# Kernel tuning notes

Measured on AMD Instinct MI355X. Metric: run time of the kernel, lower is better.

## Reference

```python
import jax, jax.numpy as jnp
import numpy as np

N_NODES = 100000
N_EDGES = 3200000
IN_FEAT = 128
HIDDEN = 32
NUM_LAYERS = 4
K = 35
NODES_PER_GRAPH = 100


def setup_inputs() -> dict:
    key = jax.random.key(0)
    ks = jax.random.split(key, 20)
    inp = {}
    inp['x'] = jax.random.normal(ks[0], (N_NODES, IN_FEAT), dtype=jnp.float32)
    inp['edge_index'] = jax.random.randint(ks[1], (2, N_EDGES), 0, N_NODES, dtype=jnp.int64)
    inp['batch'] = (jnp.arange(N_NODES, dtype=jnp.int64) // NODES_PER_GRAPH)
    # GCNConv weights (PyG: lin weight [in, out], bias [out])
    dims = [IN_FEAT] + [HIDDEN] * NUM_LAYERS
    for i in range(NUM_LAYERS):
        s = 1.0 / np.sqrt(dims[i])
        inp[f'w{i}'] = jax.random.normal(ks[2 + i], (dims[i], HIDDEN), dtype=jnp.float32) * s
        inp[f'b{i}'] = jnp.zeros((HIDDEN,), dtype=jnp.float32)
    # head: Conv1d(128->16,k=1), Conv1d(16->32,k=5), fc1(416->128), fc2(128->1)
    inp['conv1_w'] = jax.random.normal(ks[8], (16, HIDDEN * NUM_LAYERS, 1), dtype=jnp.float32) * (1.0 / np.sqrt(128))
    inp['conv1_b'] = jnp.zeros((16,), dtype=jnp.float32)
    inp['conv2_w'] = jax.random.normal(ks[9], (32, 16, 5), dtype=jnp.float32) * (1.0 / np.sqrt(16 * 5))
    inp['conv2_b'] = jnp.zeros((32,), dtype=jnp.float32)
    lin_in = 32 * (K // 2 - 4)  # 416
    inp['fc1_w'] = jax.random.normal(ks[10], (128, lin_in), dtype=jnp.float32) * (1.0 / np.sqrt(lin_in))
    inp['fc1_b'] = jnp.zeros((128,), dtype=jnp.float32)
    inp['fc2_w'] = jax.random.normal(ks[11], (1, 128), dtype=jnp.float32) * (1.0 / np.sqrt(128))
    inp['fc2_b'] = jnp.zeros((1,), dtype=jnp.float32)
    return inp


def _gcn_conv(x, w, b, src, dst, n):
    # PyG GCNConv: h = x @ W; add self-loops; sym-normalized scatter-add; + bias
    h = x @ w
    deg = jnp.ones((n,), h.dtype).at[dst].add(1.0)  # degree incl. self-loop
    dis = jax.lax.rsqrt(deg)
    coef = dis[src] * dis[dst]  # [E]
    agg = jax.ops.segment_sum(h[src] * coef[:, None], dst, num_segments=n)
    return agg + h / deg[:, None] + b  # self-loop norm = 1/deg


def reference(x, edge_index, batch, w0, b0, w1, b1, w2, b2, w3, b3,
              conv1_w, conv1_b, conv2_w, conv2_b, fc1_w, fc1_b, fc2_w, fc2_b):
    src, dst = edge_index[0], edge_index[1]
    n = x.shape[0]
    xs = []
    h = x
    for w, b in ((w0, b0), (w1, b1), (w2, b2), (w3, b3)):
        h = jnp.tanh(_gcn_conv(h, w, b, src, dst, n))
        xs.append(h)
    feat = jnp.concatenate(xs, axis=1)  # [N, 128]
    # global_sort_pool: graphs are contiguous blocks of NODES_PER_GRAPH nodes
    G = n // NODES_PER_GRAPH
    dense = feat.reshape(G, NODES_PER_GRAPH, -1)
    order = jnp.argsort(-dense[:, :, -1], axis=1)  # descending by last channel
    topk = jnp.take_along_axis(dense, order[:, :, None], axis=1)[:, :K]  # [G,K,128]
    y = topk.transpose(0, 2, 1)  # [G,128,K]
    y = jax.nn.relu(jnp.einsum('oc,gck->gok', conv1_w[:, :, 0], y) + conv1_b[None, :, None])
    L = y.shape[-1] // 2  # MaxPool1d(2), drop trailing element
    y = y[..., :L * 2].reshape(G, 16, L, 2).max(axis=-1)  # [G,16,17]
    y = jax.lax.conv_general_dilated(y, conv2_w, (1,), 'VALID',
                                     dimension_numbers=('NCH', 'OIH', 'NCH'))
    y = jax.nn.relu(y + conv2_b[None, :, None])  # [G,32,13]
    y = y.reshape(G, -1)  # [G,416]
    y = jax.nn.relu(y @ fc1_w.T + fc1_b)  # dropout is identity in eval
    return jax.nn.sigmoid(y @ fc2_w.T + fc2_b)  # [G,1]
```

## Files before the change

kernel.cpp:

```cpp
#include <hip/hip_runtime.h>
#include <hip/hip_fp16.h>
#include <math.h>

#define N_NODES 100000
#define N_EDGES 3200000
#define HIDDEN 32
#define K_TOP 35
#define NPG 100
#define N_GRAPHS 1000

#define BSHIFT 9
#define NLOC 512
#define NBUCK 196
#define CAP 17408
#define NBB 1024
#define BIN_CHUNK 13


__global__ void k_bin(const int* __restrict__ src, const int* __restrict__ dst,
                      int* __restrict__ bcnt, unsigned int* __restrict__ bdata) {
    __shared__ int h[NBUCK];
    __shared__ int lbase[NBUCK];
    __shared__ int lcur[NBUCK];
    int t = threadIdx.x;
    for (int i = t; i < NBUCK; i += 256) { h[i] = 0; lcur[i] = 0; }
    __syncthreads();
    int base = blockIdx.x * (256 * BIN_CHUNK);
    int ss[BIN_CHUNK], ds[BIN_CHUNK];
#pragma unroll
    for (int k = 0; k < BIN_CHUNK; k++) {
        int e = base + k * 256 + t;
        if (e < N_EDGES) {
            ss[k] = src[e];
            ds[k] = dst[e];
            atomicAdd(&h[ds[k] >> BSHIFT], 1);
        } else ds[k] = -1;
    }
    __syncthreads();
    for (int i = t; i < NBUCK; i += 256)
        lbase[i] = h[i] ? atomicAdd(&bcnt[i], h[i]) : 0;
    __syncthreads();
#pragma unroll
    for (int k = 0; k < BIN_CHUNK; k++) {
        int d = ds[k];
        if (d >= 0) {
            int bk = d >> BSHIFT;
            int pos = atomicAdd(&lcur[bk], 1);
            bdata[bk * CAP + lbase[bk] + pos] =
                ((unsigned int)ss[k] << BSHIFT) | (unsigned int)(d & (NLOC - 1));
        }
    }
}

__global__ void k_build(const unsigned int* __restrict__ bdata, const int* __restrict__ bcnt,
                        int2* __restrict__ rc, float* __restrict__ dis,
                        int* __restrict__ csr) {
    __shared__ int h[NLOC];
    __shared__ int sd[NLOC];
    __shared__ int rp[NLOC];
    __shared__ int cur[NLOC];
    int b = blockIdx.x, t = threadIdx.x;
    if (t < NLOC) h[t] = 0;
    __syncthreads();
    int r0 = b * CAP, r1 = r0 + bcnt[b];
    for (int i = r0 + t; i < r1; i += 1024)
        atomicAdd(&h[bdata[i] & (NLOC - 1)], 1);
    __syncthreads();
    int v = (t < NLOC) ? h[t] : 0;
    if (t < NLOC) sd[t] = v;
    __syncthreads();
    for (int off = 1; off < NLOC; off <<= 1) {
        int x = (t >= off && t < NLOC) ? sd[t - off] : 0;
        __syncthreads();
        if (t < NLOC) sd[t] += x;
        __syncthreads();
    }
    if (t < NLOC) {
        int excl = sd[t] - v;
        int node = (b << BSHIFT) + t;
        rp[t] = r0 + excl;
        cur[t] = 0;
        if (node < N_NODES) {
            rc[node] = make_int2(r0 + excl, v);
            dis[node] = rsqrtf((float)(v + 1));
        }
    }
    __syncthreads();
    for (int i = r0 + t; i < r1; i += 1024) {
        unsigned int u = bdata[i];
        int loc = u & (NLOC - 1);
        int pos = atomicAdd(&cur[loc], 1);
        csr[rp[loc] + pos] = (int)(u >> BSHIFT);
    }
}


__global__ void k_mm0(const float* __restrict__ in, const float* __restrict__ w,
                      const float* __restrict__ dis, char* __restrict__ hs) {
    __shared__ float wl[128 * HIDDEN];
    int t = threadIdx.x;
    for (int i = t; i < 128 * HIDDEN; i += 256) wl[i] = w[i];
    __syncthreads();
    int n0 = blockIdx.x * 512 + t;
    int n1 = n0 + 256;
    bool has0 = n0 < N_NODES, has1 = n1 < N_NODES;
    int m0 = has0 ? n0 : 0, m1 = has1 ? n1 : 0;
    const float* r0p = in + (size_t)m0 * 128;
    const float* r1p = in + (size_t)m1 * 128;
    float acc0[HIDDEN], acc1[HIDDEN];
#pragma unroll
    for (int o = 0; o < HIDDEN; o++) { acc0[o] = 0.f; acc1[o] = 0.f; }
    for (int c4 = 0; c4 < 32; c4++) {
        float4 va = *(const float4*)(r0p + c4 * 4);
        float4 vb = *(const float4*)(r1p + c4 * 4);
        float xa[4] = {va.x, va.y, va.z, va.w};
        float xb[4] = {vb.x, vb.y, vb.z, vb.w};
#pragma unroll
        for (int k = 0; k < 4; k++) {
            const float* wr = &wl[(c4 * 4 + k) * HIDDEN];
#pragma unroll
            for (int o = 0; o < HIDDEN; o++) {
                float wv = wr[o];
                acc0[o] += xa[k] * wv;
                acc1[o] += xb[k] * wv;
            }
        }
    }
    if (has0) {
        float d = dis[m0];
        float4* hr = (float4*)(hs + (size_t)m0 * 64);
#pragma unroll
        for (int qq = 0; qq < 4; qq++) {
            __half2 p[4];
#pragma unroll
            for (int k = 0; k < 4; k++)
                p[k] = __floats2half2_rn(acc0[8 * qq + 2 * k] * d, acc0[8 * qq + 2 * k + 1] * d);
            hr[qq] = *(float4*)p;
        }
    }
    if (has1) {
        float d = dis[m1];
        float4* hr = (float4*)(hs + (size_t)m1 * 64);
#pragma unroll
        for (int qq = 0; qq < 4; qq++) {
            __half2 p[4];
#pragma unroll
            for (int k = 0; k < 4; k++)
                p[k] = __floats2half2_rn(acc1[8 * qq + 2 * k] * d, acc1[8 * qq + 2 * k + 1] * d);
            hr[qq] = *(float4*)p;
        }
    }
}

__global__ void k_agg(const float4* __restrict__ hs4, const float* __restrict__ dis,
                      const int2* __restrict__ rc, const int* __restrict__ csr_src,
                      const float* __restrict__ bias,
                      float* __restrict__ feat, int col_off,
                      const float* __restrict__ wnext, char* __restrict__ hsn) {
    __shared__ float wl[32 * 33];
    __shared__ float tv[8][36];
    int tt = threadIdx.x;
    if (wnext) {
        for (int i = tt; i < 1024; i += 256)
            wl[(i >> 5) * 33 + (i & 31)] = wnext[i];
    }
    __syncthreads();
    int n = (blockIdx.x * 256 + tt) >> 5;
    int c = tt & 31;
    int r = c & 3;
    int ph = c >> 2;
    int slot = tt >> 5;
    int2 rcv = rc[n];
    int start = rcv.x, m = rcv.y;
    float d = dis[n];
    float4 sv = hs4[(size_t)n * 4 + r];
    float aA[8] = {0.f, 0.f, 0.f, 0.f, 0.f, 0.f, 0.f, 0.f};
    float aB[8] = {0.f, 0.f, 0.f, 0.f, 0.f, 0.f, 0.f, 0.f};

    for (int base = 0; base < m; base += 32) {
        int e = base + c;
        int idx = (e < m) ? __builtin_nontemporal_load(csr_src + start + e) : N_NODES;
        int id0 = __shfl(idx, ph, 32);
        int id1 = __shfl(idx, 8 + ph, 32);
        int id2 = __shfl(idx, 16 + ph, 32);
        int id3 = __shfl(idx, 24 + ph, 32);
        float4 g0 = hs4[(size_t)id0 * 4 + r];
        float4 g1 = hs4[(size_t)id1 * 4 + r];
        float4 g2 = hs4[(size_t)id2 * 4 + r];
        float4 g3 = hs4[(size_t)id3 * 4 + r];
        const __half2* h0 = (const __half2*)&g0;
        const __half2* h1 = (const __half2*)&g1;
        const __half2* h2 = (const __half2*)&g2;
        const __half2* h3 = (const __half2*)&g3;
        float2 f;
#pragma unroll
        for (int j = 0; j < 4; j++) {
            f = __half22float2(h0[j]); aA[2 * j] += f.x; aA[2 * j + 1] += f.y;
        }
#pragma unroll
        for (int j = 0; j < 4; j++) {
            f = __half22float2(h1[j]); aB[2 * j] += f.x; aB[2 * j + 1] += f.y;
        }
#pragma unroll
        for (int j = 0; j < 4; j++) {
            f = __half22float2(h2[j]); aA[2 * j] += f.x; aA[2 * j + 1] += f.y;
        }
#pragma unroll
        for (int j = 0; j < 4; j++) {
            f = __half22float2(h3[j]); aB[2 * j] += f.x; aB[2 * j + 1] += f.y;
        }
    }
    float s[8];
#pragma unroll
    for (int k = 0; k < 8; k++) {
        float v = aA[k] + aB[k];
        v += __shfl_xor(v, 4);
        v += __shfl_xor(v, 8);
        v += __shfl_xor(v, 16);
        s[k] = v;
    }
    float s01 = (ph & 1) ? s[1] : s[0];
    float s23 = (ph & 1) ? s[3] : s[2];
    float s45 = (ph & 1) ? s[5] : s[4];
    float s67 = (ph & 1) ? s[7] : s[6];
    float s03 = (ph & 2) ? s23 : s01;
    float s47 = (ph & 2) ? s67 : s45;
    float sp  = (ph & 4) ? s47 : s03;
    const __half2* sh = (const __half2*)&sv;
    __half2 q01 = (ph & 2) ? sh[1] : sh[0];
    __half2 q23 = (ph & 2) ? sh[3] : sh[2];
    __half2 qq  = (ph & 4) ? q23 : q01;
    float self = (ph & 1) ? __high2float(qq) : __low2float(qq);
    float bv = bias[8 * r + ph];
    float ov = tanhf(d * (sp + self) + bv);
    __builtin_nontemporal_store(ov, &feat[(size_t)n * 128 + col_off + 8 * r + ph]);
    if (wnext) {
        tv[slot][8 * r + ph] = ov;
        __builtin_amdgcn_wave_barrier();
        float o = 0.f;
#pragma unroll 8
        for (int k = 0; k < 32; k++)
            o += tv[slot][k] * wl[k * 33 + c];
        o *= d;
        float oh = __shfl_xor(o, 1);
        if ((c & 1) == 0) {
            __half2 pck = __floats2half2_rn(o, oh);
            *(__half2*)(hsn + (size_t)n * 64 + (size_t)c * 2) = pck;
        }
    }
}


__global__ void __launch_bounds__(256, 4)
k_head(const float* __restrict__ feat,
       const float* __restrict__ c1w, const float* __restrict__ c1b,
       const float* __restrict__ c2w, const float* __restrict__ c2b,
       const float* __restrict__ f1w, const float* __restrict__ f1b,
       const float* __restrict__ f2w, const float* __restrict__ f2b,
       float* __restrict__ out) {
    __shared__ float vals[NPG];
    __shared__ int sel[K_TOP];
    __shared__ float tk[K_TOP * 132];
    __shared__ float wl1[16 * 129];
    __shared__ float y1[16][36];
    __shared__ float y2[16][17];
    __shared__ float y3[416];
    __shared__ float y4[128];
    __shared__ float r2[128];
    int g = blockIdx.x, t = threadIdx.x;
    const float* fg = feat + (size_t)g * NPG * 128;

    for (int i = t; i < 2048; i += 256)
        wl1[(i >> 7) * 129 + (i & 127)] = c1w[i];
    if (t < NPG) vals[t] = fg[t * 128 + 127];
    __syncthreads();
    if (t < NPG) {
        float v = vals[t];
        int r = 0;
        for (int j = 0; j < NPG; j++) {
            float u = vals[j];
            r += (u > v) || (u == v && j < t);
        }
        if (r < K_TOP) sel[r] = t;
    }
    __syncthreads();
    for (int i = t; i < K_TOP * 32; i += 256) {
        int k = i >> 5, c4 = i & 31;
        *(float4*)&tk[k * 132 + 4 * c4] = *(const float4*)&fg[sel[k] * 128 + 4 * c4];
    }
    __syncthreads();
    for (int i = t; i < 16 * K_TOP; i += 256) {
        int o = i & 15, k = i >> 4;
        float s = c1b[o];
        const float* wr = &wl1[o * 129];
        const float* xr = &tk[k * 132];
#pragma unroll 8
        for (int c = 0; c < 128; c++) s += wr[c] * xr[c];
        y1[o][k] = fmaxf(s, 0.f);
    }
    __syncthreads();
    for (int i = t; i < 16 * 17; i += 256) {
        int o = i & 15, l = i >> 4;
        y2[o][l] = fmaxf(y1[o][2 * l], y1[o][2 * l + 1]);
    }
    __syncthreads();
    for (int idx = t; idx < 32 * 13; idx += 256) {
        int o2 = idx / 13, ttp = idx - o2 * 13;
        float s = c2b[o2];
        const float* wr = c2w + o2 * 80;
#pragma unroll
        for (int i = 0; i < 16; i++)
#pragma unroll
            for (int j = 0; j < 5; j++) s += wr[i * 5 + j] * y2[i][ttp + j];
        y3[idx] = fmaxf(s, 0.f);
    }
    __syncthreads();
    {
        int o = t >> 1, h = t & 1;
        const float4* wr4 = (const float4*)(f1w + o * 416) + h * 52;
        const float* yb = y3 + h * 208;
        float s = 0.f;
#pragma unroll 4
        for (int i = 0; i < 52; i++) {
            float4 w4 = wr4[i];
            s += w4.x * yb[4 * i] + w4.y * yb[4 * i + 1] +
                 w4.z * yb[4 * i + 2] + w4.w * yb[4 * i + 3];
        }
        s += __shfl_xor(s, 1);
        if (h == 0) y4[o] = fmaxf(s + f1b[o], 0.f);
    }
    __syncthreads();
    if (t < 128) r2[t] = f2w[t] * y4[t];
    __syncthreads();
    for (int off = 64; off > 0; off >>= 1) {
        if (t < off) r2[t] += r2[t + off];
        __syncthreads();
    }
    if (t == 0) out[g] = 1.0f / (1.0f + expf(-(r2[0] + f2b[0])));
}


static inline size_t alignup(size_t x) { return (x + 255) & ~(size_t)255; }

extern "C" void kernel_launch(void* const* d_in, const int* in_sizes, int n_in,
                              void* d_out, int out_size, void* d_ws, size_t ws_size,
                              hipStream_t stream) {
    const float* x    = (const float*)d_in[0];
    const int*   ei   = (const int*)d_in[1];
    const int*   srcp = ei;
    const int*   dstp = ei + N_EDGES;
    const float* w0 = (const float*)d_in[3];
    const float* b0 = (const float*)d_in[4];
    const float* w1 = (const float*)d_in[5];
    const float* b1 = (const float*)d_in[6];
    const float* w2 = (const float*)d_in[7];
    const float* b2 = (const float*)d_in[8];
    const float* w3 = (const float*)d_in[9];
    const float* b3 = (const float*)d_in[10];
    const float* c1w = (const float*)d_in[11];
    const float* c1b = (const float*)d_in[12];
    const float* c2w = (const float*)d_in[13];
    const float* c2b = (const float*)d_in[14];
    const float* f1w = (const float*)d_in[15];
    const float* f1b = (const float*)d_in[16];
    const float* f2w = (const float*)d_in[17];
    const float* f2b = (const float*)d_in[18];
    float* out = (float*)d_out;

    char* p = (char*)d_ws;
    int2* rcv    = (int2*)p; p += alignup(sizeof(int2) * N_NODES);
    float* dis   = (float*)p; p += alignup(sizeof(float) * N_NODES);
    int* bcnt    = (int*)p; p += alignup(sizeof(int) * NBUCK);
    int* csr     = (int*)p; p += alignup(sizeof(int) * (size_t)NBUCK * CAP);
    char* U = p;
    unsigned int* bdata = (unsigned int*)U;
    char* hsA = U;
    char* hsB = U + alignup((size_t)N_NODES * 64 + 64);
    size_t usz = alignup(sizeof(unsigned int) * (size_t)NBUCK * CAP);
    float* feat = (float*)(U + usz);

    const int NB_M = (N_NODES + 511) / 512;
    const int NB_A = (N_NODES * 32) / 256;

    hipMemsetAsync(bcnt, 0, sizeof(int) * NBUCK, stream);
    k_bin<<<NBB, 256, 0, stream>>>(srcp, dstp, bcnt, bdata);
    k_build<<<NBUCK, 1024, 0, stream>>>(bdata, bcnt, rcv, dis, csr);

    hipMemsetAsync(hsA + (size_t)N_NODES * 64, 0, 64, stream);
    hipMemsetAsync(hsB + (size_t)N_NODES * 64, 0, 64, stream);

    k_mm0<<<NB_M, 256, 0, stream>>>(x, w0, dis, hsA);
    k_agg<<<NB_A, 256, 0, stream>>>((const float4*)hsA, dis, rcv, csr, b0,
                                    feat, 0, w1, hsB);
    k_agg<<<NB_A, 256, 0, stream>>>((const float4*)hsB, dis, rcv, csr, b1,
                                    feat, 32, w2, hsA);
    k_agg<<<NB_A, 256, 0, stream>>>((const float4*)hsA, dis, rcv, csr, b2,
                                    feat, 64, w3, hsB);
    k_agg<<<NB_A, 256, 0, stream>>>((const float4*)hsB, dis, rcv, csr, b3,
                                    feat, 96, (const float*)nullptr, (char*)nullptr);

    k_head<<<N_GRAPHS, 256, 0, stream>>>(feat, c1w, c1b, c2w, c2b,
                                         f1w, f1b, f2w, f2b, out);
}
```

Measured before the change: 446.1 us.

## Replace bucketed CSR build with global atomic count-scan-fill construction

```diff
diff --git a/kernel.cpp b/kernel.cpp
--- a/kernel.cpp
+++ b/kernel.cpp
@@ -9,88 +9,73 @@
 #define NPG 100
 #define N_GRAPHS 1000
 
-#define BSHIFT 9
-#define NLOC 512
-#define NBUCK 196
-#define CAP 17408
-#define NBB 1024
-#define BIN_CHUNK 13
-
-
-__global__ void k_bin(const int* __restrict__ src, const int* __restrict__ dst,
-                      int* __restrict__ bcnt, unsigned int* __restrict__ bdata) {
-    __shared__ int h[NBUCK];
-    __shared__ int lbase[NBUCK];
-    __shared__ int lcur[NBUCK];
+#define NB_CNT 3125
+#define NB_SCAN 391
+
+
+__global__ void k_cnt(const int* __restrict__ dst, int* __restrict__ cnt) {
+    int base = blockIdx.x * 1024 + threadIdx.x;
+#pragma unroll
+    for (int k = 0; k < 4; k++)
+        atomicAdd(&cnt[dst[base + k * 256]], 1);
+}
+
+__global__ void k_scan1(const int* __restrict__ cnt, int* __restrict__ tmp,
+                        int* __restrict__ bsum) {
+    __shared__ int sd[256];
+    int b = blockIdx.x, t = threadIdx.x;
+    int i = b * 256 + t;
+    int v = (i < N_NODES) ? cnt[i] : 0;
+    sd[t] = v;
+    __syncthreads();
+    for (int off = 1; off < 256; off <<= 1) {
+        int x = (t >= off) ? sd[t - off] : 0;
+        __syncthreads();
+        sd[t] += x;
+        __syncthreads();
+    }
+    if (i < N_NODES) tmp[i] = sd[t] - v;
+    if (t == 255) bsum[b] = sd[255];
+}
+
+__global__ void k_scan2(int* __restrict__ bsum) {
+    __shared__ int sd[512];
     int t = threadIdx.x;
-    for (int i = t; i < NBUCK; i += 256) { h[i] = 0; lcur[i] = 0; }
-    __syncthreads();
-    int base = blockIdx.x * (256 * BIN_CHUNK);
-    int ss[BIN_CHUNK], ds[BIN_CHUNK];
-#pragma unroll
-    for (int k = 0; k < BIN_CHUNK; k++) {
-        int e = base + k * 256 + t;
-        if (e < N_EDGES) {
-            ss[k] = src[e];
-            ds[k] = dst[e];
-            atomicAdd(&h[ds[k] >> BSHIFT], 1);
-        } else ds[k] = -1;
-    }
-    __syncthreads();
-    for (int i = t; i < NBUCK; i += 256)
-        lbase[i] = h[i] ? atomicAdd(&bcnt[i], h[i]) : 0;
-    __syncthreads();
-#pragma unroll
-    for (int k = 0; k < BIN_CHUNK; k++) {
-        int d = ds[k];
-        if (d >= 0) {
-            int bk = d >> BSHIFT;
-            int pos = atomicAdd(&lcur[bk], 1);
-            bdata[bk * CAP + lbase[bk] + pos] =
-                ((unsigned int)ss[k] << BSHIFT) | (unsigned int)(d & (NLOC - 1));
-        }
-    }
-}
-
-__global__ void k_build(const unsigned int* __restrict__ bdata, const int* __restrict__ bcnt,
-                        int2* __restrict__ rc, float* __restrict__ dis,
-                        int* __restrict__ csr) {
-    __shared__ int h[NLOC];
-    __shared__ int sd[NLOC];
-    __shared__ int rp[NLOC];
-    __shared__ int cur[NLOC];
+    int v = (t < NB_SCAN) ? bsum[t] : 0;
+    sd[t] = v;
+    __syncthreads();
+    for (int off = 1; off < 512; off <<= 1) {
+        int x = (t >= off) ? sd[t - off] : 0;
+        __syncthreads();
+        sd[t] += x;
+        __syncthreads();
+    }
+    if (t < NB_SCAN) bsum[t] = sd[t] - v;
+}
+
+__global__ void k_scan3(const int* __restrict__ cnt, const int* __restrict__ tmp,
+                        const int* __restrict__ bsum, int2* __restrict__ rc,
+                        float* __restrict__ dis) {
     int b = blockIdx.x, t = threadIdx.x;
-    if (t < NLOC) h[t] = 0;
-    __syncthreads();
-    int r0 = b * CAP, r1 = r0 + bcnt[b];
-    for (int i = r0 + t; i < r1; i += 1024)
-        atomicAdd(&h[bdata[i] & (NLOC - 1)], 1);
-    __syncthreads();
-    int v = (t < NLOC) ? h[t] : 0;
-    if (t < NLOC) sd[t] = v;
-    __syncthreads();
-    for (int off = 1; off < NLOC; off <<= 1) {
-        int x = (t >= off && t < NLOC) ? sd[t - off] : 0;
-        __syncthreads();
-        if (t < NLOC) sd[t] += x;
-        __syncthreads();
-    }
-    if (t < NLOC) {
-        int excl = sd[t] - v;
-        int node = (b << BSHIFT) + t;
-        rp[t] = r0 + excl;
-        cur[t] = 0;
-        if (node < N_NODES) {
-            rc[node] = make_int2(r0 + excl, v);
-            dis[node] = rsqrtf((float)(v + 1));
-        }
-    }
-    __syncthreads();
-    for (int i = r0 + t; i < r1; i += 1024) {
-        unsigned int u = bdata[i];
-        int loc = u & (NLOC - 1);
-        int pos = atomicAdd(&cur[loc], 1);
-        csr[rp[loc] + pos] = (int)(u >> BSHIFT);
+    int i = b * 256 + t;
+    if (i < N_NODES) {
+        int c = cnt[i];
+        rc[i] = make_int2(tmp[i] + bsum[b], c);
+        dis[i] = rsqrtf((float)(c + 1));
+    }
+}
+
+__global__ void k_fill(const int* __restrict__ src, const int* __restrict__ dst,
+                       const int2* __restrict__ rc, int* __restrict__ cur,
+                       int* __restrict__ csr) {
+    int base = blockIdx.x * 1024 + threadIdx.x;
+#pragma unroll
+    for (int k = 0; k < 4; k++) {
+        int e = base + k * 256;
+        int d = dst[e];
+        int s = src[e];
+        int pos = atomicAdd(&cur[d], 1);
+        csr[rc[d].x + pos] = s;
     }
 }
 
@@ -173,13 +158,12 @@
     int2 rcv = rc[n];
     int start = rcv.x, m = rcv.y;
     float d = dis[n];
-    float4 sv = hs4[(size_t)n * 4 + r];
     float aA[8] = {0.f, 0.f, 0.f, 0.f, 0.f, 0.f, 0.f, 0.f};
     float aB[8] = {0.f, 0.f, 0.f, 0.f, 0.f, 0.f, 0.f, 0.f};
 
     for (int base = 0; base < m; base += 32) {
         int e = base + c;
-        int idx = (e < m) ? __builtin_nontemporal_load(csr_src + start + e) : N_NODES;
+        int idx = (e < m) ? csr_src[start + e] : N_NODES;
         int id0 = __shfl(idx, ph, 32);
         int id1 = __shfl(idx, 8 + ph, 32);
         int id2 = __shfl(idx, 16 + ph, 32);
@@ -226,6 +210,7 @@
     float s03 = (ph & 2) ? s23 : s01;
     float s47 = (ph & 2) ? s67 : s45;
     float sp  = (ph & 4) ? s47 : s03;
+    float4 sv = hs4[(size_t)n * 4 + r];
     const __half2* sh = (const __half2*)&sv;
     __half2 q01 = (ph & 2) ? sh[1] : sh[0];
     __half2 q23 = (ph & 2) ? sh[3] : sh[2];
@@ -368,23 +353,26 @@
     float* out = (float*)d_out;
 
     char* p = (char*)d_ws;
+    int* cnt     = (int*)p; p += alignup(sizeof(int) * 2 * N_NODES);
+    int* cur     = cnt + N_NODES;
+    int* tmp     = (int*)p; p += alignup(sizeof(int) * N_NODES);
+    int* bsum    = (int*)p; p += alignup(sizeof(int) * 512);
     int2* rcv    = (int2*)p; p += alignup(sizeof(int2) * N_NODES);
     float* dis   = (float*)p; p += alignup(sizeof(float) * N_NODES);
-    int* bcnt    = (int*)p; p += alignup(sizeof(int) * NBUCK);
-    int* csr     = (int*)p; p += alignup(sizeof(int) * (size_t)NBUCK * CAP);
-    char* U = p;
-    unsigned int* bdata = (unsigned int*)U;
-    char* hsA = U;
-    char* hsB = U + alignup((size_t)N_NODES * 64 + 64);
-    size_t usz = alignup(sizeof(unsigned int) * (size_t)NBUCK * CAP);
-    float* feat = (float*)(U + usz);
+    int* csr     = (int*)p; p += alignup(sizeof(int) * (size_t)N_EDGES);
+    char* hsA    = p; p += alignup((size_t)N_NODES * 64 + 64);
+    char* hsB    = p; p += alignup((size_t)N_NODES * 64 + 64);
+    float* feat  = (float*)p;
 
     const int NB_M = (N_NODES + 511) / 512;
     const int NB_A = (N_NODES * 32) / 256;
 
-    hipMemsetAsync(bcnt, 0, sizeof(int) * NBUCK, stream);
-    k_bin<<<NBB, 256, 0, stream>>>(srcp, dstp, bcnt, bdata);
-    k_build<<<NBUCK, 1024, 0, stream>>>(bdata, bcnt, rcv, dis, csr);
+    hipMemsetAsync(cnt, 0, sizeof(int) * 2 * N_NODES, stream);
+    k_cnt<<<NB_CNT, 256, 0, stream>>>(dstp, cnt);
+    k_scan1<<<NB_SCAN, 256, 0, stream>>>(cnt, tmp, bsum);
+    k_scan2<<<1, 512, 0, stream>>>(bsum);
+    k_scan3<<<NB_SCAN, 256, 0, stream>>>(cnt, tmp, bsum, rcv, dis);
+    k_fill<<<NB_CNT, 256, 0, stream>>>(srcp, dstp, rcv, cur, csr);
 
     hipMemsetAsync(hsA + (size_t)N_NODES * 64, 0, 64, stream);
     hipMemsetAsync(hsB + (size_t)N_NODES * 64, 0, 64, stream);
```

After: 641.7 us. 1.44x slower.
